# Optimization experiments

Hardware: AMD Instinct MI355X
Metric: run time of the kernel (lower is better)

Reference implementation:

```python
import math
import jax, jax.numpy as jnp
import numpy as np

T = 4096          # sequence length
H = 2048          # hidden_size
I = 8192          # intermediate_size = 4*H
LAYER_ID = 1
N_LAYERS = 24
EPS = 1e-5        # layer_norm_epsilon


def setup_inputs() -> dict:
    key = jax.random.key(0)
    ks = jax.random.split(key, 8)
    s = 1.0 / math.sqrt(H)
    si = 1.0 / math.sqrt(I)
    r0 = LAYER_ID / (N_LAYERS - 1)          # ratio_0_to_1
    r1 = 1.0 - LAYER_ID / N_LAYERS          # ratio_1_to_almost_0
    h = jnp.arange(H, dtype=jnp.float32)
    x = h / H
    time_decay = -5.0 + 8.0 * (h / (H - 1)) ** (0.7 + 1.3 * r0)
    zigzag = 0.5 * ((jnp.arange(1, H + 1) % 3).astype(jnp.float32) - 1.0)
    time_first = jnp.full((H,), math.log(0.3), jnp.float32) + zigzag
    tm_key = x ** r1
    tm_value = tm_key + 0.3 * r0
    tm_recep = x ** (0.5 * r1)
    return {
        "hidden": jax.random.normal(ks[0], (T, H), jnp.float32),
        "att_sx": jnp.zeros((H,), jnp.float32),
        "att_aa": jnp.zeros((H,), jnp.float32),
        "att_bb": jnp.zeros((H,), jnp.float32),
        "att_pp": jnp.full((H,), -1e30, jnp.float32),  # log-space -inf init
        "ffd_sx": jnp.zeros((H,), jnp.float32),
        "ln1_scale": jnp.ones((H,), jnp.float32),
        "ln1_bias": jnp.zeros((H,), jnp.float32),
        "ln2_scale": jnp.ones((H,), jnp.float32),
        "ln2_bias": jnp.zeros((H,), jnp.float32),
        "time_decay": time_decay.astype(jnp.float32),
        "time_first": time_first,
        "tm_key": tm_key.astype(jnp.float32),
        "tm_value": tm_value.astype(jnp.float32),
        "tm_recep": tm_recep.astype(jnp.float32),
        "Wk": jax.random.normal(ks[1], (H, H), jnp.float32) * s,
        "Wv": jax.random.normal(ks[2], (H, H), jnp.float32) * s,
        "Wr": jax.random.normal(ks[3], (H, H), jnp.float32) * s,
        "Wo": jax.random.normal(ks[4], (H, H), jnp.float32) * s,
        "ffn_tm_key": (x ** r1).astype(jnp.float32),
        "ffn_tm_recep": (x ** (0.5 * r1)).astype(jnp.float32),
        "Wfk": jax.random.normal(ks[5], (H, I), jnp.float32) * s,
        "Wfr": jax.random.normal(ks[6], (H, H), jnp.float32) * s,
        "Wfv": jax.random.normal(ks[7], (I, H), jnp.float32) * si,
    }


def _ln(x, scale, bias):
    mu = jnp.mean(x, axis=-1, keepdims=True)
    var = jnp.mean(jnp.square(x - mu), axis=-1, keepdims=True)
    return (x - mu) * jax.lax.rsqrt(var + EPS) * scale + bias


def _block(hidden, att_sx, att_aa, att_bb, att_pp, ffd_sx,
           ln1_scale, ln1_bias, ln2_scale, ln2_bias,
           time_decay, time_first, tm_key, tm_value, tm_recep,
           Wk, Wv, Wr, Wo, ffn_tm_key, ffn_tm_recep, Wfk, Wfr, Wfv):
    # ---- attention (WKV) sub-block ----
    x1 = _ln(hidden, ln1_scale, ln1_bias)               # [T,H]
    c_x = jnp.concatenate((att_sx[None, :], x1[:-1, :]), axis=0)  # token shift
    kx = x1 * tm_key + c_x * (1.0 - tm_key)
    vx = x1 * tm_value + c_x * (1.0 - tm_value)
    rx = x1 * tm_recep + c_x * (1.0 - tm_recep)
    r = jax.nn.sigmoid(rx @ Wr)                         # [T,H]
    k = kx @ Wk
    v = vx @ Wv
    w_decay = -jnp.exp(time_decay)                      # [H]

    def step(carry, kv):
        aa, bb, pp = carry
        kk, vv = kv
        ww = time_first + kk
        p = jnp.maximum(pp, ww)
        e1 = jnp.exp(pp - p)
        e2 = jnp.exp(ww - p)
        out_t = (e1 * aa + e2 * vv) / (e1 * bb + e2)
        ww2 = w_decay + pp
        p2 = jnp.maximum(ww2, kk)
        e1b = jnp.exp(ww2 - p2)
        e2b = jnp.exp(kk - p2)
        return (e1b * aa + e2b * vv, e1b * bb + e2b, p2), out_t

    (aa, bb, pp), cx = jax.lax.scan(step, (att_aa, att_bb, att_pp), (k, v))
    attention = x1 + (r * cx) @ Wo                      # inner residual (as in source)
    hidden2 = hidden + attention

    # ---- feed-forward (channel-mix) sub-block ----
    x2 = _ln(hidden2, ln2_scale, ln2_bias)
    sx2 = jnp.concatenate((ffd_sx[None, :], x2[:-1, :]), axis=0)
    fk = x2 * ffn_tm_key + sx2 * (1.0 - ffn_tm_key)
    fr = x2 * ffn_tm_recep + sx2 * (1.0 - ffn_tm_recep)
    rr = jax.nn.sigmoid(fr @ Wfr)
    kk2 = jnp.square(jax.nn.relu(fk @ Wfk))             # [T,I]
    ffn = rr * (kk2 @ Wfv)
    out = hidden2 + ffn
    return out, x1[-1, :], aa, bb, pp, x2[-1, :]


def reference(hidden, att_sx, att_aa, att_bb, att_pp, ffd_sx,
              ln1_scale, ln1_bias, ln2_scale, ln2_bias,
              time_decay, time_first, tm_key, tm_value, tm_recep,
              Wk, Wv, Wr, Wo, ffn_tm_key, ffn_tm_recep, Wfk, Wfr, Wfv):
    return _block(hidden, att_sx, att_aa, att_bb, att_pp, ffd_sx,
                  ln1_scale, ln1_bias, ln2_scale, ln2_bias,
                  time_decay, time_first, tm_key, tm_value, tm_recep,
                  Wk, Wv, Wr, Wo, ffn_tm_key, ffn_tm_recep, Wfk, Wfr, Wfv)
```

## Files before the change

### kernel.cpp

```cpp
#include <hip/hip_runtime.h>

#define T_SEQ 4096
#define HD 2048
#define ID 8192
#define LN_EPS 1e-5f
#define NCH 64
#define CHL 64
#define CHSZ ((size_t)NCH * HD)

typedef __attribute__((ext_vector_type(4))) float f32x4;
typedef __attribute__((ext_vector_type(8))) short short8;
typedef __attribute__((ext_vector_type(4))) unsigned short ushort4v;

#define GLB(p) ((const __attribute__((address_space(1))) void*)(p))
#define LDSP(p) ((__attribute__((address_space(3))) void*)(p))

__device__ __forceinline__ unsigned short f2bf(float f) {
  union { float f; unsigned int u; } x; x.f = f;
  unsigned int r = x.u + 0x7fffu + ((x.u >> 16) & 1u);
  return (unsigned short)(r >> 16);
}
__device__ __forceinline__ float bf2f(unsigned short u) {
  union { unsigned int i; float f; } x; x.i = ((unsigned int)u) << 16;
  return x.f;
}

__global__ void k_wt(const float* __restrict__ W, unsigned short* __restrict__ Wt,
                     int Nfull, int k_base, int n_base, int Kout) {
  __shared__ float tile[64][65];
  int tx = threadIdx.x, ty = threadIdx.y;
  int n0 = blockIdx.x * 64, k0 = blockIdx.y * 64;
#pragma unroll
  for (int j = 0; j < 8; ++j) {
    int k = ty + 8 * j;
    tile[k][tx] = W[(size_t)(k_base + k0 + k) * Nfull + n_base + n0 + tx];
  }
  __syncthreads();
#pragma unroll
  for (int j = 0; j < 8; ++j) {
    int n = ty + 8 * j;
    Wt[(size_t)(n0 + n) * Kout + k0 + tx] = f2bf(tile[tx][n]);
  }
}

__global__ void k_ln(const float* __restrict__ x, const float* __restrict__ sc,
                     const float* __restrict__ bi, unsigned short* __restrict__ y,
                     float* __restrict__ lastrow) {
  int row = blockIdx.x, tid = threadIdx.x;
  const float* xr = x + (size_t)row * HD;
  f32x4 v0 = *(const f32x4*)(xr + tid * 4);
  f32x4 v1 = *(const f32x4*)(xr + 1024 + tid * 4);
  float s = 0.f, s2 = 0.f;
#pragma unroll
  for (int q = 0; q < 4; ++q) { s += v0[q] + v1[q]; s2 += v0[q] * v0[q] + v1[q] * v1[q]; }
#pragma unroll
  for (int o = 32; o; o >>= 1) { s += __shfl_xor(s, o); s2 += __shfl_xor(s2, o); }
  __shared__ float red[8];
  int wv = tid >> 6;
  if ((tid & 63) == 0) { red[wv] = s; red[4 + wv] = s2; }
  __syncthreads();
  if (tid == 0) {
    float a = red[0] + red[1] + red[2] + red[3];
    float b = red[4] + red[5] + red[6] + red[7];
    float mu = a * (1.f / HD);
    float var = b * (1.f / HD) - mu * mu;
    red[0] = mu; red[1] = rsqrtf(var + LN_EPS);
  }
  __syncthreads();
  float mu = red[0], rs = red[1];
  f32x4 s0 = *(const f32x4*)(sc + tid * 4), s1 = *(const f32x4*)(sc + 1024 + tid * 4);
  f32x4 b0 = *(const f32x4*)(bi + tid * 4), b1 = *(const f32x4*)(bi + 1024 + tid * 4);
  float o0[4], o1[4];
  ushort4v y0, y1;
#pragma unroll
  for (int q = 0; q < 4; ++q) {
    o0[q] = (v0[q] - mu) * rs * s0[q] + b0[q];
    o1[q] = (v1[q] - mu) * rs * s1[q] + b1[q];
    y0[q] = f2bf(o0[q]); y1[q] = f2bf(o1[q]);
  }
  unsigned short* yr = y + (size_t)row * HD;
  *(ushort4v*)(yr + tid * 4) = y0;
  *(ushort4v*)(yr + 1024 + tid * 4) = y1;
  if (row == T_SEQ - 1) {
#pragma unroll
    for (int q = 0; q < 4; ++q) {
      lastrow[tid * 4 + q] = o0[q];
      lastrow[1024 + tid * 4 + q] = o1[q];
    }
  }
}

__global__ void k_mix_att(const unsigned short* __restrict__ x1, const float* __restrict__ sx,
                          const float* __restrict__ tk, const float* __restrict__ tv,
                          const float* __restrict__ tr,
                          unsigned short* __restrict__ kx, unsigned short* __restrict__ vx,
                          unsigned short* __restrict__ rx) {
  size_t idx = ((size_t)blockIdx.x * 256 + threadIdx.x) * 4;
  int h = (int)(idx & (HD - 1));
  ushort4v xu = *(const ushort4v*)(x1 + idx);
  f32x4 x, c;
#pragma unroll
  for (int q = 0; q < 4; ++q) x[q] = bf2f(xu[q]);
  if (idx >= HD) {
    ushort4v cu = *(const ushort4v*)(x1 + idx - HD);
#pragma unroll
    for (int q = 0; q < 4; ++q) c[q] = bf2f(cu[q]);
  } else {
    c = *(const f32x4*)(sx + h);
  }
  f32x4 a = *(const f32x4*)(tk + h);
  f32x4 b = *(const f32x4*)(tv + h);
  f32x4 r = *(const f32x4*)(tr + h);
  ushort4v ok, ov, orr;
#pragma unroll
  for (int q = 0; q < 4; ++q) {
    ok[q] = f2bf(x[q] * a[q] + c[q] * (1.f - a[q]));
    ov[q] = f2bf(x[q] * b[q] + c[q] * (1.f - b[q]));
    orr[q] = f2bf(x[q] * r[q] + c[q] * (1.f - r[q]));
  }
  *(ushort4v*)(kx + idx) = ok;
  *(ushort4v*)(vx + idx) = ov;
  *(ushort4v*)(rx + idx) = orr;
}

__global__ void k_mix_ffn(const unsigned short* __restrict__ x2, const float* __restrict__ sx,
                          const float* __restrict__ tk, const float* __restrict__ tr,
                          unsigned short* __restrict__ fk, unsigned short* __restrict__ fr) {
  size_t idx = ((size_t)blockIdx.x * 256 + threadIdx.x) * 4;
  int h = (int)(idx & (HD - 1));
  ushort4v xu = *(const ushort4v*)(x2 + idx);
  f32x4 x, c;
#pragma unroll
  for (int q = 0; q < 4; ++q) x[q] = bf2f(xu[q]);
  if (idx >= HD) {
    ushort4v cu = *(const ushort4v*)(x2 + idx - HD);
#pragma unroll
    for (int q = 0; q < 4; ++q) c[q] = bf2f(cu[q]);
  } else {
    c = *(const f32x4*)(sx + h);
  }
  f32x4 a = *(const f32x4*)(tk + h);
  f32x4 r = *(const f32x4*)(tr + h);
  ushort4v ok, orr;
#pragma unroll
  for (int q = 0; q < 4; ++q) {
    ok[q] = f2bf(x[q] * a[q] + c[q] * (1.f - a[q]));
    orr[q] = f2bf(x[q] * r[q] + c[q] * (1.f - r[q]));
  }
  *(ushort4v*)(fk + idx) = ok;
  *(ushort4v*)(fr + idx) = orr;
}

__global__ void k_scan1(const unsigned short* __restrict__ kb,
                        const unsigned short* __restrict__ vb,
                        const float* __restrict__ td, float* __restrict__ scr) {
  int c = blockIdx.x >> 3;
  int h = (blockIdx.x & 7) * 256 + threadIdx.x;
  float wd = -__expf(td[h]);
  float a = 0.f, b = 0.f, p = -1e30f;
  size_t base = (size_t)c * CHL * HD + h;
#pragma unroll 4
  for (int u = 0; u < CHL; ++u) {
    float kk = bf2f(kb[base]), vv = bf2f(vb[base]);
    base += HD;
    float ww2 = wd + p;
    float p2 = fmaxf(ww2, kk);
    float e1 = __expf(ww2 - p2), e2 = __expf(kk - p2);
    a = e1 * a + e2 * vv;
    b = e1 * b + e2;
    p = p2;
  }
  size_t i = (size_t)c * HD + h;
  scr[i] = a;
  scr[CHSZ + i] = b;
  scr[2 * CHSZ + i] = p;
}

__global__ void k_scan2(const float* __restrict__ scr, float* __restrict__ stscr,
                        const float* __restrict__ aa0, const float* __restrict__ bb0,
                        const float* __restrict__ pp0, const float* __restrict__ td,
                        float* __restrict__ st) {
  int h = blockIdx.x * 256 + threadIdx.x;
  float aa = aa0[h], bb = bb0[h], pp = pp0[h];
  float wdL = -__expf(td[h]) * (float)CHL;
  for (int c = 0; c < NCH; ++c) {
    size_t i = (size_t)c * HD + h;
    stscr[i] = aa;
    stscr[CHSZ + i] = bb;
    stscr[2 * CHSZ + i] = pp;
    float ca = scr[i], cb = scr[CHSZ + i], cp = scr[2 * CHSZ + i];
    float ww2 = wdL + pp;
    float p2 = fmaxf(ww2, cp);
    float e1 = __expf(ww2 - p2), e2 = __expf(cp - p2);
    aa = e1 * aa + e2 * ca;
    bb = e1 * bb + e2 * cb;
    pp = p2;
  }
  st[HD + h] = aa;
  st[2 * HD + h] = bb;
  st[3 * HD + h] = pp;
}

__global__ void k_scan3(const unsigned short* __restrict__ kb,
                        const unsigned short* __restrict__ vb,
                        const unsigned short* __restrict__ rb,
                        const float* __restrict__ tf_, const float* __restrict__ td,
                        const float* __restrict__ stscr, unsigned short* __restrict__ rcx) {
  int c = blockIdx.x >> 3;
  int h = (blockIdx.x & 7) * 256 + threadIdx.x;
  size_t i0 = (size_t)c * HD + h;
  float aa = stscr[i0], bb = stscr[CHSZ + i0], pp = stscr[2 * CHSZ + i0];
  float tf = tf_[h];
  float wd = -__expf(td[h]);
  size_t base = (size_t)c * CHL * HD + h;
#pragma unroll 4
  for (int u = 0; u < CHL; ++u) {
    float kk = bf2f(kb[base]), vv = bf2f(vb[base]), rv = bf2f(rb[base]);
    float ww = tf + kk;
    float p = fmaxf(pp, ww);
    float e1 = __expf(pp - p), e2 = __expf(ww - p);
    float cx = (e1 * aa + e2 * vv) / (e1 * bb + e2);
    rcx[base] = f2bf(rv * cx);
    float ww2 = wd + pp;
    float p2 = fmaxf(ww2, kk);
    float e1b = __expf(ww2 - p2), e2b = __expf(kk - p2);
    aa = e1b * aa + e2b * vv;
    bb = e1b * bb + e2b;
    pp = p2;
    base += HD;
  }
}

#define MFMA_Q(mh, nh, bset)                                                   \
  _Pragma("unroll") for (int i_ = 0; i_ < 4; ++i_)                             \
  _Pragma("unroll") for (int j_ = 0; j_ < 2; ++j_)                             \
  _Pragma("unroll") for (int ks_ = 0; ks_ < 2; ++ks_)                          \
    acc[(mh)*4 + i_][(nh)*2 + j_] = __builtin_amdgcn_mfma_f32_16x16x32_bf16(   \
        aS[i_ * 2 + ks_], bset[j_ * 2 + ks_], acc[(mh)*4 + i_][(nh)*2 + j_], 0, 0, 0);

#define RD_A(mh)                                                               \
  { const char* pa_ = Ab + arow0 + (mh)*8192;                                  \
    aS[0] = *(const short8*)(pa_ + 0 * 2048 + swz0);                           \
    aS[1] = *(const short8*)(pa_ + 0 * 2048 + swz1);                           \
    aS[2] = *(const short8*)(pa_ + 1 * 2048 + swz0);                           \
    aS[3] = *(const short8*)(pa_ + 1 * 2048 + swz1);                           \
    aS[4] = *(const short8*)(pa_ + 2 * 2048 + swz0);                           \
    aS[5] = *(const short8*)(pa_ + 2 * 2048 + swz1);                           \
    aS[6] = *(const short8*)(pa_ + 3 * 2048 + swz0);                           \
    aS[7] = *(const short8*)(pa_ + 3 * 2048 + swz1); }

#define RD_B(arr, nh)                                                          \
  { const char* pb_ = Bb + brow0 + (nh)*4096;                                  \
    arr[0] = *(const short8*)(pb_ + 0 * 2048 + swz0);                          \
    arr[1] = *(const short8*)(pb_ + 0 * 2048 + swz1);                          \
    arr[2] = *(const short8*)(pb_ + 1 * 2048 + swz0);                          \
    arr[3] = *(const short8*)(pb_ + 1 * 2048 + swz1); }

template <int EPI>
__global__ __launch_bounds__(512, 2) void k_gemm256(
    const unsigned short* __restrict__ A, const unsigned short* __restrict__ A1,
    const unsigned short* __restrict__ A2,
    const unsigned short* __restrict__ Bt, const unsigned short* __restrict__ Bt1,
    const unsigned short* __restrict__ Bt2,
    int M, int N, int K, int lda, int ldb,
    unsigned short* __restrict__ Cb, unsigned short* __restrict__ Cb1,
    unsigned short* __restrict__ Cb2) {
  if (blockIdx.z == 1) { A = A1; Bt = Bt1; Cb = Cb1; }
  else if (blockIdx.z == 2) { A = A2; Bt = Bt2; Cb = Cb2; }
  __shared__ char lds[131072];
  int tid = threadIdx.x;
  int wid = tid >> 6, lane = tid & 63;
  int row_l = lane & 15, kg = lane >> 4;
  int warp_m = wid >> 2, warp_n = wid & 3;
  int m0 = blockIdx.x * 256, n0 = blockIdx.y * 256;

  f32x4 acc[8][4];
#pragma unroll
  for (int i = 0; i < 8; ++i)
#pragma unroll
    for (int j = 0; j < 4; ++j)
#pragma unroll
      for (int q = 0; q < 4; ++q) acc[i][j][q] = 0.f;

  int srow = tid >> 3;
  int schunk = (tid & 7) ^ (srow & 7);
  const unsigned short* Asrc = A + (size_t)(m0 + srow) * lda + schunk * 8;
  const unsigned short* Bsrc = Bt + (size_t)(n0 + srow) * ldb + schunk * 8;
  char* ldsw = lds + wid * 1024;

  auto STAGE_A = [&](int d, int kt) {
#pragma unroll
    for (int h = 0; h < 2; ++h) {
      const unsigned short* s = Asrc + (size_t)(h * 128) * lda + kt;
      char* dst = ldsw + d * 65536 + h * 16384;
      __builtin_amdgcn_global_load_lds(GLB(s), LDSP(dst), 16, 0, 0);
      __builtin_amdgcn_global_load_lds(GLB(s + (size_t)64 * lda), LDSP(dst + 8192), 16, 0, 0);
    }
  };
  auto STAGE_B = [&](int d, int kt) {
#pragma unroll
    for (int h = 0; h < 2; ++h) {
      const unsigned short* s = Bsrc + (size_t)(h * 128) * ldb + kt;
      char* dst = ldsw + d * 65536 + 32768 + h * 16384;
      __builtin_amdgcn_global_load_lds(GLB(s), LDSP(dst), 16, 0, 0);
      __builtin_amdgcn_global_load_lds(GLB(s + (size_t)64 * ldb), LDSP(dst + 8192), 16, 0, 0);
    }
  };

  int swz0 = ((kg) ^ (row_l & 7)) << 4;
  int swz1 = ((4 + kg) ^ (row_l & 7)) << 4;
  int arow0 = (warp_m * 128 + row_l) * 128;
  int brow0 = (warp_n * 64 + row_l) * 128;

  short8 aS[8], b0[4], b1[4];
  int nt = K >> 6;
  STAGE_A(0, 0);
  STAGE_B(0, 0);

#pragma unroll 1
  for (int t = 0; t < nt; ++t) {
    int d = t & 1;
    const char* Ab = lds + d * 65536;
    const char* Bb = lds + d * 65536 + 32768;
    bool pre = (t + 1 < nt);
    int kn = (t + 1) << 6;
    if (pre) {
      STAGE_A(d ^ 1, kn);
      asm volatile("s_waitcnt vmcnt(4)" ::: "memory");
    } else {
      asm volatile("s_waitcnt vmcnt(0)" ::: "memory");
    }
    __builtin_amdgcn_s_barrier();
    RD_A(0)
    RD_B(b0, 0)
    asm volatile("s_waitcnt lgkmcnt(0)" ::: "memory");
    __builtin_amdgcn_s_setprio(1);
    MFMA_Q(0, 0, b0)
    __builtin_amdgcn_s_setprio(0);
    __builtin_amdgcn_s_barrier();
    if (pre) STAGE_B(d ^ 1, kn);
    RD_B(b1, 1)
    asm volatile("s_waitcnt lgkmcnt(0)" ::: "memory");
    __builtin_amdgcn_s_setprio(1);
    MFMA_Q(0, 1, b1)
    __builtin_amdgcn_s_setprio(0);
    __builtin_amdgcn_s_barrier();
    RD_A(1)
    asm volatile("s_waitcnt lgkmcnt(0)" ::: "memory");
    __builtin_amdgcn_s_setprio(1);
    MFMA_Q(1, 1, b1)
    __builtin_amdgcn_s_setprio(0);
    __builtin_amdgcn_s_barrier();
    __builtin_amdgcn_s_setprio(1);
    MFMA_Q(1, 0, b0)
    __builtin_amdgcn_s_setprio(0);
    __builtin_amdgcn_s_barrier();
  }

#pragma unroll
  for (int i = 0; i < 8; ++i) {
#pragma unroll
    for (int j = 0; j < 4; ++j) {
#pragma unroll
      for (int q = 0; q < 4; ++q) {
        int r = m0 + warp_m * 128 + i * 16 + kg * 4 + q;
        int c = n0 + warp_n * 64 + j * 16 + row_l;
        size_t idx = (size_t)r * N + c;
        float val = acc[i][j][q];
        if (EPI == 2) { float t2 = val > 0.f ? val * val : 0.f; Cb[idx] = f2bf(t2); }
        if (EPI == 8) {
          float o = (blockIdx.z == 2) ? 1.f / (1.f + __expf(-val)) : val;
          Cb[idx] = f2bf(o);
        }
      }
    }
  }
}

template <int EPI, int SWAP>
__global__ __launch_bounds__(512) void k_gemmB(
    const unsigned short* __restrict__ A, const unsigned short* __restrict__ Bt,
    int M, int N, int K, int lda, float* __restrict__ C,
    unsigned short* __restrict__ Cb, const float* __restrict__ E0,
    const unsigned short* __restrict__ E1b, const unsigned short* __restrict__ E0b) {
  __shared__ char lds[147456];
  int tid = threadIdx.x;
  int wid = tid >> 6, lane = tid & 63;
  int row_l = lane & 15, kg = lane >> 4;
  int warp_m = wid >> 2, warp_n = wid & 3;
  int bm = SWAP ? blockIdx.y : blockIdx.x;
  int bn = SWAP ? blockIdx.x : blockIdx.y;
  int m0 = bm * 128, n0 = bn * 256;

  f32x4 acc[4][4];
#pragma unroll
  for (int i = 0; i < 4; ++i)
#pragma unroll
    for (int j = 0; j < 4; ++j)
#pragma unroll
      for (int q = 0; q < 4; ++q) acc[i][j][q] = 0.f;

  int srow = tid >> 3;
  int schunk = (tid & 7) ^ (srow & 7);
  const unsigned short* Asrc = A + (size_t)(m0 + srow) * lda + schunk * 8;
  const unsigned short* Bsrc = Bt + (size_t)(n0 + srow) * K + schunk * 8;
  int wsw = wid * 1024;

  auto STAGE_P1 = [&](int d, int kt) {
    char* base = lds + d * 49152;
    __builtin_amdgcn_global_load_lds(GLB(Asrc + kt), LDSP(base + wsw), 16, 0, 0);
    __builtin_amdgcn_global_load_lds(GLB(Asrc + (size_t)64 * lda + kt),
                                     LDSP(base + 8192 + wsw), 16, 0, 0);
    __builtin_amdgcn_global_load_lds(GLB(Bsrc + kt), LDSP(base + 16384 + wsw), 16, 0, 0);
  };
  auto STAGE_P2 = [&](int d, int kt) {
    char* base = lds + d * 49152;
#pragma unroll
    for (int h = 1; h < 4; ++h)
      __builtin_amdgcn_global_load_lds(GLB(Bsrc + (size_t)(h * 64) * K + kt),
                                       LDSP(base + 16384 + h * 8192 + wsw), 16, 0, 0);
  };

  int swz0 = ((kg) ^ (row_l & 7)) << 4;
  int swz1 = ((4 + kg) ^ (row_l & 7)) << 4;
  int arow0 = (warp_m * 64 + row_l) * 128;
  int brow0 = (warp_n * 64 + row_l) * 128;

  short8 aS[8], b0[4], b1[4];
  int nt = K >> 6;
  STAGE_P1(0, 0); STAGE_P2(0, 0);
  STAGE_P1(1, 64); STAGE_P2(1, 64);

#pragma unroll 1
  for (int t = 0; t < nt; ++t) {
    int d = t % 3;
    const char* Ab = lds + d * 49152;
    const char* Bb = lds + d * 49152 + 16384;
    int b2 = t + 2 < nt ? (t + 2) % 3 : 0;
    int k2 = (t + 2) << 6;
    if (t + 2 < nt) {
      STAGE_P1(b2, k2);
      asm volatile("s_waitcnt vmcnt(9)" ::: "memory");
    } else if (t + 1 < nt) {
      asm volatile("s_waitcnt vmcnt(6)" ::: "memory");
    } else {
      asm volatile("s_waitcnt vmcnt(0)" ::: "memory");
    }
    __builtin_amdgcn_s_barrier();
    RD_A(0)
    RD_B(b0, 0)
    asm volatile("s_waitcnt lgkmcnt(0)" ::: "memory");
    __builtin_amdgcn_s_setprio(1);
    MFMA_Q(0, 0, b0)
    __builtin_amdgcn_s_setprio(0);
    __builtin_amdgcn_s_barrier();
    if (t + 2 < nt) STAGE_P2(b2, k2);
    RD_B(b1, 1)
    asm volatile("s_waitcnt lgkmcnt(0)" ::: "memory");
    __builtin_amdgcn_s_setprio(1);
    MFMA_Q(0, 1, b1)
    __builtin_amdgcn_s_setprio(0);
    __builtin_amdgcn_s_barrier();
  }

#pragma unroll
  for (int i = 0; i < 4; ++i) {
#pragma unroll
    for (int j = 0; j < 4; ++j) {
#pragma unroll
      for (int q = 0; q < 4; ++q) {
        int r = m0 + warp_m * 64 + i * 16 + kg * 4 + q;
        int c = n0 + warp_n * 64 + j * 16 + row_l;
        size_t idx = (size_t)r * N + c;
        float val = acc[i][j][q];
        if (EPI == 3) C[idx] = val + E0[idx] + bf2f(E1b[idx]);
        if (EPI == 6) Cb[idx] = f2bf(1.f / (1.f + __expf(-val)));
        if (EPI == 7) C[idx] += bf2f(E0b[idx]) * val;
      }
    }
  }
}

extern "C" void kernel_launch(void* const* d_in, const int* in_sizes, int n_in,
                              void* d_out, int out_size, void* d_ws, size_t ws_size,
                              hipStream_t stream) {
  (void)in_sizes; (void)n_in; (void)out_size; (void)ws_size;
  const float* hidden     = (const float*)d_in[0];
  const float* att_sx     = (const float*)d_in[1];
  const float* att_aa     = (const float*)d_in[2];
  const float* att_bb     = (const float*)d_in[3];
  const float* att_pp     = (const float*)d_in[4];
  const float* ffd_sx     = (const float*)d_in[5];
  const float* ln1_s      = (const float*)d_in[6];
  const float* ln1_b      = (const float*)d_in[7];
  const float* ln2_s      = (const float*)d_in[8];
  const float* ln2_b      = (const float*)d_in[9];
  const float* time_decay = (const float*)d_in[10];
  const float* time_first = (const float*)d_in[11];
  const float* tm_key     = (const float*)d_in[12];
  const float* tm_value   = (const float*)d_in[13];
  const float* tm_recep   = (const float*)d_in[14];
  const float* Wk         = (const float*)d_in[15];
  const float* Wv         = (const float*)d_in[16];
  const float* Wr         = (const float*)d_in[17];
  const float* Wo         = (const float*)d_in[18];
  const float* ffn_tm_key = (const float*)d_in[19];
  const float* ffn_tm_rec = (const float*)d_in[20];
  const float* Wfk        = (const float*)d_in[21];
  const float* Wfr        = (const float*)d_in[22];
  const float* Wfv        = (const float*)d_in[23];
  float* out = (float*)d_out;
  float* st = out + (size_t)T_SEQ * HD;

  const size_t MB8 = (size_t)HD * HD * 2;
  const size_t PG = (size_t)T_SEQ * HD * 2;
  char* w = (char*)d_ws;
  unsigned short* s0 = (unsigned short*)(w);
  unsigned short* s1 = (unsigned short*)(w + MB8);
  unsigned short* s2 = (unsigned short*)(w + 2 * MB8);
  unsigned short* s3 = (unsigned short*)(w + 3 * MB8);
  char* pA = w + 4 * MB8;
  char* pB = pA + PG;
  char* pC = pB + PG;
  char* pD = pC + PG;
  char* pE = pD + PG;
  char* pF = pE + PG;

  unsigned short* kx   = (unsigned short*)pA;
  unsigned short* vx   = (unsigned short*)pB;
  unsigned short* rx   = (unsigned short*)pC;
  unsigned short* kbf  = (unsigned short*)pD;
  unsigned short* x1bf = (unsigned short*)pE;
  unsigned short* vbf  = (unsigned short*)pF;
  unsigned short* rbf  = (unsigned short*)out;
  unsigned short* rcx  = (unsigned short*)pC;
  unsigned short* x2bf = (unsigned short*)pD;
  unsigned short* fk   = (unsigned short*)pF;
  unsigned short* fr   = (unsigned short*)pB;
  unsigned short* rr   = (unsigned short*)pA;
  unsigned short* kk2  = (unsigned short*)pB;
  float* scr   = (float*)s0;
  float* stscr = (float*)s1;

  dim3 tb64(64, 8);
  dim3 wg64(HD / 64, HD / 64);
  dim3 gBs(HD / 256, T_SEQ / 128);

  k_wt<<<wg64, tb64, 0, stream>>>(Wk, s0, HD, 0, 0, HD);
  k_wt<<<wg64, tb64, 0, stream>>>(Wv, s1, HD, 0, 0, HD);
  k_wt<<<wg64, tb64, 0, stream>>>(Wr, s2, HD, 0, 0, HD);
  k_wt<<<wg64, tb64, 0, stream>>>(Wo, s3, HD, 0, 0, HD);
  k_ln<<<T_SEQ, 256, 0, stream>>>(hidden, ln1_s, ln1_b, x1bf, st);
  k_mix_att<<<T_SEQ * HD / 1024, 256, 0, stream>>>(x1bf, att_sx, tm_key, tm_value, tm_recep,
                                                   kx, vx, rx);
  k_gemm256<8><<<dim3(T_SEQ / 256, HD / 256, 3), 512, 0, stream>>>(
      kx, vx, rx, s0, s1, s2, T_SEQ, HD, HD, HD, HD, kbf, vbf, rbf);
  k_scan1<<<NCH * 8, 256, 0, stream>>>(kbf, vbf, time_decay, scr);
  k_scan2<<<HD / 256, 256, 0, stream>>>(scr, stscr, att_aa, att_bb, att_pp, time_decay, st);
  k_scan3<<<NCH * 8, 256, 0, stream>>>(kbf, vbf, rbf, time_first, time_decay, stscr, rcx);
  k_gemmB<3, 1><<<gBs, 512, 0, stream>>>(rcx, s3, T_SEQ, HD, HD, HD, out, nullptr,
                                         hidden, x1bf, nullptr);

  k_ln<<<T_SEQ, 256, 0, stream>>>(out, ln2_s, ln2_b, x2bf, st + 4 * HD);
  k_mix_ffn<<<T_SEQ * HD / 1024, 256, 0, stream>>>(x2bf, ffd_sx, ffn_tm_key, ffn_tm_rec,
                                                   fk, fr);
  k_wt<<<wg64, tb64, 0, stream>>>(Wfr, s3, HD, 0, 0, HD);
  k_gemmB<6, 1><<<gBs, 512, 0, stream>>>(fr, s3, T_SEQ, HD, HD, HD, nullptr, rr,
                                         nullptr, nullptr, nullptr);
  for (int q = 0; q < 4; ++q)
    k_wt<<<wg64, tb64, 0, stream>>>(Wfk, s0 + (size_t)q * 2048 * 2048, ID, 0, q * 2048, HD);
  k_gemm256<2><<<dim3(T_SEQ / 256, ID / 256), 512, 0, stream>>>(
      fk, nullptr, nullptr, s0, nullptr, nullptr, T_SEQ, ID, HD, HD, HD,
      kk2, nullptr, nullptr);
  for (int q = 0; q < 4; ++q)
    k_wt<<<dim3(HD / 64, HD / 64), tb64, 0, stream>>>(Wfv, s0 + (size_t)q * 2048, HD,
                                                      q * 2048, 0, ID);
  k_gemmB<7, 1><<<gBs, 512, 0, stream>>>(kk2, s0, T_SEQ, HD, ID, ID, out, nullptr,
                                         nullptr, nullptr, rr);
}
```

Measured before the change: 649.8 us.

## Split-K the final FFN down-projection into two halves plus reduction kernel

```diff
diff --git a/kernel.cpp b/kernel.cpp
--- a/kernel.cpp
+++ b/kernel.cpp
@@ -10,6 +10,7 @@
 
 typedef __attribute__((ext_vector_type(4))) float f32x4;
 typedef __attribute__((ext_vector_type(8))) short short8;
+typedef __attribute__((ext_vector_type(8))) unsigned short ushort8v;
 typedef __attribute__((ext_vector_type(4))) unsigned short ushort4v;
 
 #define GLB(p) ((const __attribute__((address_space(1))) void*)(p))
@@ -36,11 +37,10 @@
     tile[k][tx] = W[(size_t)(k_base + k0 + k) * Nfull + n_base + n0 + tx];
   }
   __syncthreads();
-#pragma unroll
-  for (int j = 0; j < 8; ++j) {
-    int n = ty + 8 * j;
-    Wt[(size_t)(n0 + n) * Kout + k0 + tx] = f2bf(tile[tx][n]);
-  }
+  ushort8v v;
+#pragma unroll
+  for (int q = 0; q < 8; ++q) v[q] = f2bf(tile[ty * 8 + q][tx]);
+  *(ushort8v*)&Wt[(size_t)(n0 + tx) * Kout + k0 + ty * 8] = v;
 }
 
 __global__ void k_ln(const float* __restrict__ x, const float* __restrict__ sc,
@@ -231,6 +231,19 @@
   }
 }
 
+__global__ void k_fvred(float* __restrict__ out, const unsigned short* __restrict__ rr,
+                        const unsigned short* __restrict__ p0,
+                        const unsigned short* __restrict__ p1) {
+  size_t i = ((size_t)blockIdx.x * 256 + threadIdx.x) * 4;
+  f32x4 o = *(f32x4*)(out + i);
+  ushort4v r = *(const ushort4v*)(rr + i);
+  ushort4v a = *(const ushort4v*)(p0 + i);
+  ushort4v b = *(const ushort4v*)(p1 + i);
+#pragma unroll
+  for (int q = 0; q < 4; ++q) o[q] += bf2f(r[q]) * (bf2f(a[q]) + bf2f(b[q]));
+  *(f32x4*)(out + i) = o;
+}
+
 #define MFMA_Q(mh, nh, bset)                                                   \
   _Pragma("unroll") for (int i_ = 0; i_ < 4; ++i_)                             \
   _Pragma("unroll") for (int j_ = 0; j_ < 2; ++j_)                             \
@@ -265,8 +278,14 @@
     int M, int N, int K, int lda, int ldb,
     unsigned short* __restrict__ Cb, unsigned short* __restrict__ Cb1,
     unsigned short* __restrict__ Cb2) {
-  if (blockIdx.z == 1) { A = A1; Bt = Bt1; Cb = Cb1; }
-  else if (blockIdx.z == 2) { A = A2; Bt = Bt2; Cb = Cb2; }
+  int koff = 0;
+  if (EPI == 10) {
+    koff = blockIdx.z * K;
+    if (blockIdx.z) Cb = Cb1;
+  } else {
+    if (blockIdx.z == 1) { A = A1; Bt = Bt1; Cb = Cb1; }
+    else if (blockIdx.z == 2) { A = A2; Bt = Bt2; Cb = Cb2; }
+  }
   __shared__ char lds[131072];
   int tid = threadIdx.x;
   int wid = tid >> 6, lane = tid & 63;
@@ -284,8 +303,8 @@
 
   int srow = tid >> 3;
   int schunk = (tid & 7) ^ (srow & 7);
-  const unsigned short* Asrc = A + (size_t)(m0 + srow) * lda + schunk * 8;
-  const unsigned short* Bsrc = Bt + (size_t)(n0 + srow) * ldb + schunk * 8;
+  const unsigned short* Asrc = A + (size_t)(m0 + srow) * lda + koff + schunk * 8;
+  const unsigned short* Bsrc = Bt + (size_t)(n0 + srow) * ldb + koff + schunk * 8;
   char* ldsw = lds + wid * 1024;
 
   auto STAGE_A = [&](int d, int kt) {
@@ -372,6 +391,7 @@
           float o = (blockIdx.z == 2) ? 1.f / (1.f + __expf(-val)) : val;
           Cb[idx] = f2bf(o);
         }
+        if (EPI == 10) Cb[idx] = f2bf(val);
       }
     }
   }
@@ -484,7 +504,7 @@
 extern "C" void kernel_launch(void* const* d_in, const int* in_sizes, int n_in,
                               void* d_out, int out_size, void* d_ws, size_t ws_size,
                               hipStream_t stream) {
-  (void)in_sizes; (void)n_in; (void)out_size; (void)ws_size;
+  (void)in_sizes; (void)n_in; (void)out_size;
   const float* hidden     = (const float*)d_in[0];
   const float* att_sx     = (const float*)d_in[1];
   const float* att_aa     = (const float*)d_in[2];
@@ -539,8 +559,11 @@
   unsigned short* fr   = (unsigned short*)pB;
   unsigned short* rr   = (unsigned short*)pA;
   unsigned short* kk2  = (unsigned short*)pB;
+  unsigned short* pfv0 = (unsigned short*)pF;
+  unsigned short* pfv1 = (unsigned short*)(w + 4 * MB8 + 6 * PG);
   float* scr   = (float*)s0;
   float* stscr = (float*)s1;
+  bool big_ws = ws_size >= (size_t)(4 * MB8 + 7 * PG);
 
   dim3 tb64(64, 8);
   dim3 wg64(HD / 64, HD / 64);
@@ -575,6 +598,13 @@
   for (int q = 0; q < 4; ++q)
     k_wt<<<dim3(HD / 64, HD / 64), tb64, 0, stream>>>(Wfv, s0 + (size_t)q * 2048, HD,
                                                       q * 2048, 0, ID);
-  k_gemmB<7, 1><<<gBs, 512, 0, stream>>>(kk2, s0, T_SEQ, HD, ID, ID, out, nullptr,
-                                         nullptr, nullptr, rr);
-}
+  if (big_ws) {
+    k_gemm256<10><<<dim3(T_SEQ / 256, HD / 256, 2), 512, 0, stream>>>(
+        kk2, nullptr, nullptr, s0, nullptr, nullptr, T_SEQ, HD, ID / 2, ID, ID,
+        pfv0, pfv1, nullptr);
+    k_fvred<<<T_SEQ * HD / 1024, 256, 0, stream>>>(out, rr, pfv0, pfv1);
+  } else {
+    k_gemmB<7, 1><<<gBs, 512, 0, stream>>>(kk2, s0, T_SEQ, HD, ID, ID, out, nullptr,
+                                           nullptr, nullptr, rr);
+  }
+}
```

After: 657.1 us. About the same (+1.1%).
